# Performance work log

Measured on AMD Instinct MI355X. Metric: run time of the kernel, lower is better.

The kernel has to match this reference:

```python
import jax, jax.numpy as jnp
import numpy as np

V, D, H, DH, P, NL, FF, NC, MAXP = 32000, 512, 8, 64, 16, 8, 2048, 4, 512
B, L = 32, 4096


def _ln(x, s, b, eps=1e-5):
    m = x.mean(-1, keepdims=True)
    v = ((x - m) ** 2).mean(-1, keepdims=True)
    return (x - m) * jax.lax.rsqrt(v + eps) * s + b


def _rope(x):
    # x: [B,S,H,Dh] -- GPT-NeoX style rotary over head dim
    S, d = x.shape[1], x.shape[-1]
    inv_freq = 1.0 / (10000.0 ** (jnp.arange(0, d, 2, dtype=jnp.float32) / d))
    freqs = jnp.arange(S, dtype=jnp.float32)[:, None] * inv_freq[None, :]  # [S,d/2]
    emb = jnp.concatenate([freqs, freqs], axis=-1)  # [S,d]
    cos = jnp.cos(emb)[None, :, None, :]
    sin = jnp.sin(emb)[None, :, None, :]
    x1, x2 = x[..., : d // 2], x[..., d // 2:]
    rot = jnp.concatenate([-x2, x1], axis=-1)
    return x * cos + rot * sin


def setup_inputs():
    key = jax.random.key(0)
    ks = jax.random.split(key, 20)
    s = 0.02
    inp = {}
    inp['inputs'] = jax.random.randint(ks[0], (B, L), 0, V, dtype=jnp.int32)
    inp['input_mask'] = jnp.ones((B, L), dtype=jnp.float32)
    inp['emb'] = jax.random.normal(ks[1], (V, D)) * s
    inp['conv_w'] = jax.random.normal(ks[2], (D, D, P)) * s  # [out, in, kernel]
    inp['conv_b'] = jnp.zeros((D,))
    inp['pos'] = jax.random.normal(ks[3], (MAXP, D)) * s
    inp['cls'] = jax.random.normal(ks[4], (1, 1, D))
    inp['Wq'] = jax.random.normal(ks[5], (NL, D, D)) * s
    inp['bq'] = jnp.zeros((NL, D))
    inp['Wk'] = jax.random.normal(ks[6], (NL, D, D)) * s
    inp['bk'] = jnp.zeros((NL, D))
    inp['Wv'] = jax.random.normal(ks[7], (NL, D, D)) * s
    inp['bv'] = jnp.zeros((NL, D))
    inp['Wo'] = jax.random.normal(ks[8], (NL, D, D)) * s
    inp['bo'] = jnp.zeros((NL, D))
    inp['ln1_s'] = jnp.ones((NL, D))
    inp['ln1_b'] = jnp.zeros((NL, D))
    inp['ln2_s'] = jnp.ones((NL, D))
    inp['ln2_b'] = jnp.zeros((NL, D))
    inp['W1'] = jax.random.normal(ks[9], (NL, D, FF)) * s
    inp['b1'] = jnp.zeros((NL, FF))
    inp['W2'] = jax.random.normal(ks[10], (NL, FF, D)) * s
    inp['b2'] = jnp.zeros((NL, D))
    inp['lnf_s'] = jnp.ones((D,))
    inp['lnf_b'] = jnp.zeros((D,))
    inp['out_w'] = jax.random.normal(ks[11], (D, NC)) * s
    inp['out_b'] = jnp.zeros((NC,))
    return inp


def _forward(inputs, input_mask, emb, conv_w, conv_b, pos, cls, Wq, bq, Wk, bk, Wv, bv,
             Wo, bo, ln1_s, ln1_b, ln2_s, ln2_b, W1, b1, W2, b2, lnf_s, lnf_b, out_w, out_b):
    b, l = inputs.shape
    n = l // P
    x = emb[inputs]  # [B,L,D]
    # patchify conv1d (kernel == stride) == blocked reshape + einsum
    x = jnp.einsum('bnpi,oip->bno', x.reshape(b, n, P, D), conv_w) + conv_b
    x = jnp.concatenate([jnp.broadcast_to(cls, (b, 1, D)), x], axis=1)  # [B,S,D]
    S = n + 1
    x = x + pos[:S][None]
    # length mask at patch granularity: ceil((sum(mask)+1)/patch_size)
    lengths = jnp.ceil((input_mask.sum(-1) + 1.0) / P)
    lmask = (jnp.arange(S, dtype=jnp.float32)[None, :] < lengths[:, None]).astype(x.dtype)  # [B,S]
    for i in range(NL):
        q = (x @ Wq[i] + bq[i]).reshape(b, S, H, DH)
        k = (x @ Wk[i] + bk[i]).reshape(b, S, H, DH)
        v = (x @ Wv[i] + bv[i]).reshape(b, S, H, DH)
        q, k = _rope(q), _rope(k)
        qf = jax.nn.elu(q) + 1.0  # kernel feature map
        kf = (jax.nn.elu(k) + 1.0) * lmask[:, :, None, None]
        kv = jnp.einsum('bshd,bshm->bhdm', kf, v)
        z = 1.0 / (jnp.einsum('bshd,bhd->bsh', qf, kf.sum(axis=1)) + 1e-6)
        attn = jnp.einsum('bshd,bhdm,bsh->bshm', qf, kv, z).reshape(b, S, D)
        x = x + (attn @ Wo[i] + bo[i])
        x = _ln(x, ln1_s[i], ln1_b[i])
        y = jax.nn.gelu(x @ W1[i] + b1[i], approximate=False) @ W2[i] + b2[i]
        x = _ln(x + y, ln2_s[i], ln2_b[i])
    x = _ln(x, lnf_s, lnf_b)
    return x[:, 0] @ out_w + out_b  # [B, num_classes]


def reference(inputs, input_mask, emb, conv_w, conv_b, pos, cls, Wq, bq, Wk, bk, Wv, bv,
              Wo, bo, ln1_s, ln1_b, ln2_s, ln2_b, W1, b1, W2, b2, lnf_s, lnf_b, out_w, out_b):
    return _forward(inputs, input_mask, emb, conv_w, conv_b, pos, cls, Wq, bq, Wk, bk, Wv, bv,
                    Wo, bo, ln1_s, ln1_b, ln2_s, ln2_b, W1, b1, W2, b2, lnf_s, lnf_b, out_w, out_b)
```

## Files before the change

### kernel.cpp

```cpp
#include <hip/hip_runtime.h>
#include <cstdint>

typedef unsigned short u16;
typedef __attribute__((ext_vector_type(8))) short short8;
typedef __attribute__((ext_vector_type(4))) float floatx4;

typedef __attribute__((address_space(1))) void as1_void;
typedef __attribute__((address_space(3))) void as3_void;

__device__ __forceinline__ float b2f(u16 u) {
  return __uint_as_float(((unsigned int)u) << 16);
}
__device__ __forceinline__ u16 f2b(float f) {
  unsigned int x = __float_as_uint(f);
  x += 0x7fffu + ((x >> 16) & 1u);
  return (u16)(x >> 16);
}
__device__ __forceinline__ float ldf(const void* p, size_t i, int f32) {
  return f32 ? ((const float*)p)[i] : b2f(((const u16*)p)[i]);
}

__device__ __forceinline__ void gl_lds16(const u16* g, u16* l) {
  __builtin_amdgcn_global_load_lds((const as1_void*)g, (as3_void*)l, 16, 0, 0);
}

template<int EPI, bool GATHER>
__global__ __launch_bounds__(256)
void gemm_bt(const u16* __restrict__ A, const u16* __restrict__ BT,
             int M, int K, int N,
             const u16* __restrict__ bias,
             float* __restrict__ outf, u16* __restrict__ outb,
             const int* __restrict__ tok, const u16* __restrict__ emb,
             const u16* __restrict__ pos, float* __restrict__ xf, u16* __restrict__ xb)
{
  __shared__ u16 lds[16384];
  u16* Al = lds;
  u16* Bl = lds + 8192;
  const int tid  = threadIdx.x;
  const int wave = tid >> 6, lane = tid & 63;
  const int m0 = blockIdx.x * 128, n0 = blockIdx.y * 128;
  const int wy = wave & 1, wx = wave >> 1;

  floatx4 acc[4][4];
#pragma unroll
  for (int i = 0; i < 4; ++i)
#pragma unroll
    for (int j = 0; j < 4; ++j) acc[i][j] = (floatx4){0.f, 0.f, 0.f, 0.f};

  for (int k0 = 0; k0 < K; k0 += 64) {
#pragma unroll
    for (int t = 0; t < 4; ++t) {
      int slot = t * 256 + wave * 64 + lane;
      int r = slot >> 3, cp = slot & 7;
      int c = cp ^ (r & 7);
      int grow = m0 + r; if (grow >= M) grow = M - 1;
      const u16* g;
      if (GATHER) {
        int k = k0 + c * 8;
        g = emb + ((size_t)tok[grow * 16 + (k >> 9)] * 512 + (k & 511));
      } else {
        g = A + ((size_t)grow * K + k0 + c * 8);
      }
      gl_lds16(g, Al + (size_t)(t * 256 + wave * 64) * 8);
    }
#pragma unroll
    for (int t = 0; t < 4; ++t) {
      int slot = t * 256 + wave * 64 + lane;
      int r = slot >> 3, cp = slot & 7;
      int c = cp ^ (r & 7);
      const u16* g = BT + ((size_t)(n0 + r) * K + k0 + c * 8);
      gl_lds16(g, Bl + (size_t)(t * 256 + wave * 64) * 8);
    }
    __syncthreads();

#pragma unroll
    for (int ks = 0; ks < 2; ++ks) {
      short8 af[4], bfr[4];
#pragma unroll
      for (int mt = 0; mt < 4; ++mt) {
        int r = wy * 64 + mt * 16 + (lane & 15);
        int ch = ks * 4 + (lane >> 4);
        af[mt] = *(const short8*)(Al + (size_t)(r * 8 + (ch ^ (r & 7))) * 8);
      }
#pragma unroll
      for (int nt = 0; nt < 4; ++nt) {
        int r = wx * 64 + nt * 16 + (lane & 15);
        int ch = ks * 4 + (lane >> 4);
        bfr[nt] = *(const short8*)(Bl + (size_t)(r * 8 + (ch ^ (r & 7))) * 8);
      }
#pragma unroll
      for (int mt = 0; mt < 4; ++mt)
#pragma unroll
        for (int nt = 0; nt < 4; ++nt)
          acc[mt][nt] = __builtin_amdgcn_mfma_f32_16x16x32_bf16(af[mt], bfr[nt], acc[mt][nt], 0, 0, 0);
    }
    __syncthreads();
  }

  const int rb = m0 + wy * 64 + ((lane >> 4) << 2);
  const int cb = n0 + wx * 64 + (lane & 15);
#pragma unroll
  for (int mt = 0; mt < 4; ++mt) {
#pragma unroll
    for (int rr = 0; rr < 4; ++rr) {
      int row = rb + mt * 16 + rr;
      if (row >= M) continue;
#pragma unroll
      for (int nt = 0; nt < 4; ++nt) {
        int col = cb + nt * 16;
        float v = acc[mt][nt][rr] + b2f(bias[col]);
        if (EPI == 0) {
          outf[(size_t)row * N + col] = v;
        } else if (EPI == 1) {
          float gl = 0.5f * v * (1.0f + erff(v * 0.70710678118654752f));
          outb[(size_t)row * N + col] = f2b(gl);
        } else if (EPI == 3) {
          outb[(size_t)row * N + col] = f2b(v);
        } else {
          int bb = row >> 8, ss = (row & 255) + 1;
          v += b2f(pos[ss * 512 + col]);
          size_t o = ((size_t)(bb * 257 + ss)) * 512 + col;
          xf[o] = v;
          xb[o] = f2b(v);
        }
      }
    }
  }
}

__global__ void detect_kernel(const void* mask, int* flag)
{
  if (threadIdx.x == 0 && blockIdx.x == 0)
    flag[0] = (((const u16*)mask)[0] == 0) ? 1 : 0;
}

__global__ __launch_bounds__(256)
void cvt_kernel(const void* __restrict__ src, u16* __restrict__ dst, int n,
                const int* __restrict__ flag)
{
  int f = flag[0];
  int i = blockIdx.x * 256 + threadIdx.x;
  if (i < n) dst[i] = f2b(ldf(src, i, f));
}

__global__ __launch_bounds__(256)
void transpose_any(const void* __restrict__ in, size_t eoff,
                   u16* __restrict__ out, int R, int C,
                   const int* __restrict__ flag)
{
  __shared__ u16 tile[32][33];
  int f = flag[0];
  int c0 = blockIdx.x * 32, r0 = blockIdx.y * 32;
  int tx = threadIdx.x, ty = threadIdx.y;
#pragma unroll
  for (int i = 0; i < 32; i += 8)
    tile[ty + i][tx] = f2b(ldf(in, eoff + (size_t)(r0 + ty + i) * C + (c0 + tx), f));
  __syncthreads();
#pragma unroll
  for (int i = 0; i < 32; i += 8)
    out[(size_t)(c0 + ty + i) * R + (r0 + tx)] = tile[tx][ty + i];
}

__global__ __launch_bounds__(256)
void conv_repack(const void* __restrict__ w, u16* __restrict__ wt,
                 const int* __restrict__ flag)
{
  __shared__ u16 t[8192];
  int f = flag[0];
  int o = blockIdx.x, tid = threadIdx.x;
  for (int i = tid; i < 8192; i += 256)
    t[i] = f2b(ldf(w, (size_t)o * 8192 + i, f));
  __syncthreads();
  u16* dst = wt + (size_t)o * 8192;
  for (int j = tid; j < 8192; j += 256) {
    int p = j >> 9, i = j & 511;
    dst[j] = t[i * 16 + p];
  }
}

__global__ __launch_bounds__(256)
void cls_kernel(const u16* __restrict__ cls, const u16* __restrict__ pos,
                float* __restrict__ xf, u16* __restrict__ xb)
{
  int b = blockIdx.x, tid = threadIdx.x;
  for (int i = tid; i < 512; i += 256) {
    float v = b2f(cls[i]) + b2f(pos[i]);
    size_t o = ((size_t)b * 257) * 512 + i;
    xf[o] = v;
    xb[o] = f2b(v);
  }
}

__global__ __launch_bounds__(256)
void lengths_kernel(const void* __restrict__ mask, float* __restrict__ lens,
                    const int* __restrict__ flag)
{
  __shared__ float red[4];
  int f = flag[0];
  int b = blockIdx.x, tid = threadIdx.x;
  float s = 0.f;
  for (int i = tid; i < 4096; i += 256) s += ldf(mask, (size_t)b * 4096 + i, f);
#pragma unroll
  for (int o = 1; o < 64; o <<= 1) s += __shfl_xor(s, o);
  if ((tid & 63) == 0) red[tid >> 6] = s;
  __syncthreads();
  if (tid == 0) lens[b] = ceilf((red[0] + red[1] + red[2] + red[3] + 1.0f) * (1.0f / 16.0f));
}

__global__ __launch_bounds__(256)
void rope_elu(float* __restrict__ q, float* __restrict__ k, const float* __restrict__ lens)
{
  int i = blockIdx.x * 256 + threadIdx.x;
  int j = i & 31, h = (i >> 5) & 7, t = i >> 8;
  int s = t % 257, b = t / 257;
  size_t base = (size_t)t * 512 + h * 64 + j;
  float inv = __expf(-(float)j * (9.210340371976184f / 32.0f));
  float ang = (float)s * inv;
  float c, sn;
  __sincosf(ang, &sn, &c);
  float q1 = q[base], q2 = q[base + 32];
  float r1 = q1 * c - q2 * sn, r2 = q2 * c + q1 * sn;
  q[base]      = (r1 > 0.f) ? (r1 + 1.f) : __expf(r1);
  q[base + 32] = (r2 > 0.f) ? (r2 + 1.f) : __expf(r2);
  float msk = ((float)s < lens[b]) ? 1.f : 0.f;
  float k1 = k[base], k2 = k[base + 32];
  r1 = k1 * c - k2 * sn; r2 = k2 * c + k1 * sn;
  k[base]      = ((r1 > 0.f) ? (r1 + 1.f) : __expf(r1)) * msk;
  k[base + 32] = ((r2 > 0.f) ? (r2 + 1.f) : __expf(r2)) * msk;
}

__global__ __launch_bounds__(256)
void kv_kernel(const float* __restrict__ kf, const u16* __restrict__ v,
               float* __restrict__ kv, float* __restrict__ ksum)
{
  int bh = blockIdx.x, b = bh >> 3, h = bh & 7;
  int tid = threadIdx.x, d = tid & 63, mg = tid >> 6;
  float acc[16];
#pragma unroll
  for (int j = 0; j < 16; ++j) acc[j] = 0.f;
  float ks = 0.f;
  for (int s = 0; s < 257; ++s) {
    size_t base = ((size_t)(b * 257 + s)) * 512 + h * 64;
    float kfv = kf[base + d];
    const u16* vr = v + base + mg * 16;
#pragma unroll
    for (int j = 0; j < 16; ++j) acc[j] += kfv * b2f(vr[j]);
    ks += kfv;
  }
  float* kvo = kv + (size_t)bh * 4096 + d * 64 + mg * 16;
#pragma unroll
  for (int j = 0; j < 16; ++j) kvo[j] = acc[j];
  if (mg == 0) ksum[(size_t)bh * 64 + d] = ks;
}

__global__ __launch_bounds__(256)
void z_kernel(const float* __restrict__ qf, const float* __restrict__ ksum,
              float* __restrict__ z)
{
  int i = blockIdx.x * 256 + threadIdx.x;
  if (i >= 65792) return;
  int h = i & 7, t = i >> 3, b = t / 257;
  const float* qr = qf + (size_t)t * 512 + h * 64;
  const float* kr = ksum + ((size_t)b * 8 + h) * 64;
  float s = 0.f;
#pragma unroll
  for (int d = 0; d < 64; ++d) s += qr[d] * kr[d];
  z[i] = 1.0f / (s + 1e-6f);
}

__global__ __launch_bounds__(256)
void attn_kernel(const float* __restrict__ qf, const float* __restrict__ kv,
                 const float* __restrict__ z, u16* __restrict__ attn)
{
  __shared__ float kvs[4096];
  int bh = blockIdx.x, b = bh >> 3, h = bh & 7;
  int tid = threadIdx.x;
  const float* kvg = kv + (size_t)bh * 4096;
  for (int i = tid; i < 4096; i += 256) kvs[i] = kvg[i];
  __syncthreads();
  int m = tid & 63;
  for (int s = tid >> 6; s < 257; s += 4) {
    size_t base = ((size_t)(b * 257 + s)) * 512 + h * 64;
    float zz = z[(b * 257 + s) * 8 + h];
    float sum = 0.f;
#pragma unroll
    for (int d = 0; d < 64; ++d) sum += qf[base + d] * kvs[d * 64 + m];
    attn[base + m] = f2b(sum * zz);
  }
}

__global__ __launch_bounds__(256)
void ln_kernel(const float* __restrict__ xin, const float* __restrict__ add,
               const u16* __restrict__ s, const u16* __restrict__ b,
               float* __restrict__ xoutf, u16* __restrict__ xoutb)
{
  __shared__ float red[8];
  int row = blockIdx.x, tid = threadIdx.x;
  size_t base = (size_t)row * 512;
  float v0 = xin[base + tid] + add[base + tid];
  float v1 = xin[base + tid + 256] + add[base + tid + 256];
  float sum = v0 + v1, sq = v0 * v0 + v1 * v1;
#pragma unroll
  for (int o = 1; o < 64; o <<= 1) { sum += __shfl_xor(sum, o); sq += __shfl_xor(sq, o); }
  if ((tid & 63) == 0) { red[tid >> 6] = sum; red[4 + (tid >> 6)] = sq; }
  __syncthreads();
  sum = red[0] + red[1] + red[2] + red[3];
  sq  = red[4] + red[5] + red[6] + red[7];
  float mean = sum * (1.f / 512.f);
  float var  = sq * (1.f / 512.f) - mean * mean;
  float rs = rsqrtf(fmaxf(var, 0.f) + 1e-5f);
  float o0 = (v0 - mean) * rs * b2f(s[tid]) + b2f(b[tid]);
  float o1 = (v1 - mean) * rs * b2f(s[tid + 256]) + b2f(b[tid + 256]);
  xoutf[base + tid] = o0;       xoutf[base + tid + 256] = o1;
  xoutb[base + tid] = f2b(o0);  xoutb[base + tid + 256] = f2b(o1);
}

__global__ __launch_bounds__(256)
void head_kernel(const float* __restrict__ x, const u16* __restrict__ ls,
                 const u16* __restrict__ lb, const u16* __restrict__ ow,
                 const u16* __restrict__ ob, void* __restrict__ outv,
                 const int* __restrict__ flag)
{
  __shared__ float red[8];
  __shared__ float pr[4][4];
  int b = blockIdx.x, tid = threadIdx.x;
  const float* xr = x + (size_t)b * 257 * 512;
  float v0 = xr[tid], v1 = xr[tid + 256];
  float sum = v0 + v1, sq = v0 * v0 + v1 * v1;
#pragma unroll
  for (int o = 1; o < 64; o <<= 1) { sum += __shfl_xor(sum, o); sq += __shfl_xor(sq, o); }
  if ((tid & 63) == 0) { red[tid >> 6] = sum; red[4 + (tid >> 6)] = sq; }
  __syncthreads();
  sum = red[0] + red[1] + red[2] + red[3];
  sq  = red[4] + red[5] + red[6] + red[7];
  float mean = sum * (1.f / 512.f);
  float var = sq * (1.f / 512.f) - mean * mean;
  float rs = rsqrtf(fmaxf(var, 0.f) + 1e-5f);
  float o0 = (v0 - mean) * rs * b2f(ls[tid]) + b2f(lb[tid]);
  float o1 = (v1 - mean) * rs * b2f(ls[tid + 256]) + b2f(lb[tid + 256]);
  float p[4];
#pragma unroll
  for (int c = 0; c < 4; ++c)
    p[c] = o0 * b2f(ow[tid * 4 + c]) + o1 * b2f(ow[(tid + 256) * 4 + c]);
#pragma unroll
  for (int c = 0; c < 4; ++c)
#pragma unroll
    for (int o = 1; o < 64; o <<= 1) p[c] += __shfl_xor(p[c], o);
  if ((tid & 63) == 0)
#pragma unroll
    for (int c = 0; c < 4; ++c) pr[tid >> 6][c] = p[c];
  __syncthreads();
  if (tid < 4) {
    float s = pr[0][tid] + pr[1][tid] + pr[2][tid] + pr[3][tid] + b2f(ob[tid]);
    if (flag[0]) ((float*)outv)[b * 4 + tid] = s;
    else         ((u16*)outv)[b * 4 + tid] = f2b(s);
  }
}

__global__ __launch_bounds__(256)
void diag_kernel(u16* out, int n, float v)
{
  int i = blockIdx.x * 256 + threadIdx.x;
  if (i < n) out[i] = f2b(v);
}

extern "C" void kernel_launch(void* const* d_in, const int* in_sizes, int n_in,
                              void* d_out, int out_size, void* d_ws, size_t ws_size,
                              hipStream_t stream)
{
  const int*  inputs = (const int*)d_in[0];
  const void* imask  = d_in[1];
  const void* emb    = d_in[2];
  const void* conv_w = d_in[3];
  const void* conv_b = d_in[4];
  const void* pos    = d_in[5];
  const void* cls    = d_in[6];
  const void* Wq = d_in[7];  const void* bq = d_in[8];
  const void* Wk = d_in[9];  const void* bk = d_in[10];
  const void* Wv = d_in[11]; const void* bv = d_in[12];
  const void* Wo = d_in[13]; const void* bo = d_in[14];
  const void* ln1s = d_in[15]; const void* ln1b = d_in[16];
  const void* ln2s = d_in[17]; const void* ln2b = d_in[18];
  const void* W1 = d_in[19]; const void* b1 = d_in[20];
  const void* W2 = d_in[21]; const void* b2 = d_in[22];
  const void* lnfs = d_in[23]; const void* lnfb = d_in[24];
  const void* outw = d_in[25]; const void* outbb = d_in[26];

  const size_t NEED = 87500000;
  if (ws_size < NEED) {
    diag_kernel<<<(out_size + 255) / 256, 256, 0, stream>>>(
        (u16*)d_out, out_size, (float)((double)ws_size / 1048576.0));
    return;
  }
  char* p = (char*)d_ws;
  auto take = [&](size_t n) { char* r = p; p += (n + 255) & ~(size_t)255; return r; };
  u16*   WqT = (u16*)take(524288);
  u16*   WkT = (u16*)take(524288);
  u16*   WvT = (u16*)take(524288);
  u16*   WoT = (u16*)take(524288);
  u16*   W1T = (u16*)take(2097152);
  u16*   W2T = (u16*)take(2097152);
  float* xf  = (float*)take(16842752);
  u16*   xb  = (u16*)take(8421376);
  char*  arena = take(16842752ull * 2);
  float* qb    = (float*)arena;
  float* kb    = (float*)(arena + 16842752);
  u16*   embC  = (u16*)arena;
  u16*   attnb = (u16*)(arena + 16842752);
  u16*   y1    = (u16*)arena;
  char*  Cblk  = take(16842752);
  u16*   convT = (u16*)Cblk;
  u16*   vb    = (u16*)Cblk;
  float* t0    = (float*)Cblk;
  float* kvb   = (float*)take(4194304);
  float* ksumb = (float*)take(65536);
  float* zb    = (float*)take(263168);
  float* lens  = (float*)take(256);
  int*   flag  = (int*)take(256);
  u16* conv_bC = (u16*)take(1024);
  u16* posC    = (u16*)take(524288);
  u16* clsC    = (u16*)take(1024);
  u16* bqC     = (u16*)take(8192);
  u16* bkC     = (u16*)take(8192);
  u16* bvC     = (u16*)take(8192);
  u16* boC     = (u16*)take(8192);
  u16* ln1sC   = (u16*)take(8192);
  u16* ln1bC   = (u16*)take(8192);
  u16* ln2sC   = (u16*)take(8192);
  u16* ln2bC   = (u16*)take(8192);
  u16* b1C     = (u16*)take(32768);
  u16* b2C     = (u16*)take(8192);
  u16* lnfsC   = (u16*)take(1024);
  u16* lnfbC   = (u16*)take(1024);
  u16* outwC   = (u16*)take(4096);
  u16* outbC   = (u16*)take(256);

  detect_kernel<<<1, 64, 0, stream>>>(imask, flag);

  cvt_kernel<<<64000, 256, 0, stream>>>(emb, embC, 16384000, flag);
  conv_repack<<<512, 256, 0, stream>>>(conv_w, convT, flag);
  cvt_kernel<<<2, 256, 0, stream>>>(conv_b, conv_bC, 512, flag);
  cvt_kernel<<<1024, 256, 0, stream>>>(pos, posC, 262144, flag);
  cvt_kernel<<<2, 256, 0, stream>>>(cls, clsC, 512, flag);
  cvt_kernel<<<16, 256, 0, stream>>>(bq, bqC, 4096, flag);
  cvt_kernel<<<16, 256, 0, stream>>>(bk, bkC, 4096, flag);
  cvt_kernel<<<16, 256, 0, stream>>>(bv, bvC, 4096, flag);
  cvt_kernel<<<16, 256, 0, stream>>>(bo, boC, 4096, flag);
  cvt_kernel<<<16, 256, 0, stream>>>(ln1s, ln1sC, 4096, flag);
  cvt_kernel<<<16, 256, 0, stream>>>(ln1b, ln1bC, 4096, flag);
  cvt_kernel<<<16, 256, 0, stream>>>(ln2s, ln2sC, 4096, flag);
  cvt_kernel<<<16, 256, 0, stream>>>(ln2b, ln2bC, 4096, flag);
  cvt_kernel<<<64, 256, 0, stream>>>(b1, b1C, 16384, flag);
  cvt_kernel<<<16, 256, 0, stream>>>(b2, b2C, 4096, flag);
  cvt_kernel<<<2, 256, 0, stream>>>(lnfs, lnfsC, 512, flag);
  cvt_kernel<<<2, 256, 0, stream>>>(lnfb, lnfbC, 512, flag);
  cvt_kernel<<<8, 256, 0, stream>>>(outw, outwC, 2048, flag);
  cvt_kernel<<<1, 256, 0, stream>>>(outbb, outbC, 4, flag);
  lengths_kernel<<<32, 256, 0, stream>>>(imask, lens, flag);

  gemm_bt<2, true><<<dim3(64, 4), 256, 0, stream>>>(
      nullptr, convT, 8192, 8192, 512, conv_bC,
      nullptr, nullptr, inputs, embC, posC, xf, xb);
  cls_kernel<<<32, 256, 0, stream>>>(clsC, posC, xf, xb);

  for (int i = 0; i < 8; ++i) {
    const size_t o512 = (size_t)i * 262144;
    const size_t o2k  = (size_t)i * 1048576;
    transpose_any<<<dim3(16, 16), dim3(32, 8), 0, stream>>>(Wq, o512, WqT, 512, 512, flag);
    transpose_any<<<dim3(16, 16), dim3(32, 8), 0, stream>>>(Wk, o512, WkT, 512, 512, flag);
    transpose_any<<<dim3(16, 16), dim3(32, 8), 0, stream>>>(Wv, o512, WvT, 512, 512, flag);
    transpose_any<<<dim3(16, 16), dim3(32, 8), 0, stream>>>(Wo, o512, WoT, 512, 512, flag);
    transpose_any<<<dim3(64, 16), dim3(32, 8), 0, stream>>>(W1, o2k, W1T, 512, 2048, flag);
    transpose_any<<<dim3(16, 64), dim3(32, 8), 0, stream>>>(W2, o2k, W2T, 2048, 512, flag);

    gemm_bt<0, false><<<dim3(65, 4), 256, 0, stream>>>(
        xb, WqT, 8224, 512, 512, bqC + i * 512,
        qb, nullptr, nullptr, nullptr, nullptr, nullptr, nullptr);
    gemm_bt<0, false><<<dim3(65, 4), 256, 0, stream>>>(
        xb, WkT, 8224, 512, 512, bkC + i * 512,
        kb, nullptr, nullptr, nullptr, nullptr, nullptr, nullptr);
    gemm_bt<3, false><<<dim3(65, 4), 256, 0, stream>>>(
        xb, WvT, 8224, 512, 512, bvC + i * 512,
        nullptr, vb, nullptr, nullptr, nullptr, nullptr, nullptr);
    rope_elu<<<8224, 256, 0, stream>>>(qb, kb, lens);
    kv_kernel<<<256, 256, 0, stream>>>(kb, vb, kvb, ksumb);
    z_kernel<<<257, 256, 0, stream>>>(qb, ksumb, zb);
    attn_kernel<<<256, 256, 0, stream>>>(qb, kvb, zb, attnb);
    gemm_bt<0, false><<<dim3(65, 4), 256, 0, stream>>>(
        attnb, WoT, 8224, 512, 512, boC + i * 512,
        t0, nullptr, nullptr, nullptr, nullptr, nullptr, nullptr);
    ln_kernel<<<8224, 256, 0, stream>>>(xf, t0, ln1sC + i * 512, ln1bC + i * 512, xf, xb);
    gemm_bt<1, false><<<dim3(65, 16), 256, 0, stream>>>(
        xb, W1T, 8224, 512, 2048, b1C + i * 2048,
        nullptr, y1, nullptr, nullptr, nullptr, nullptr, nullptr);
    gemm_bt<0, false><<<dim3(65, 4), 256, 0, stream>>>(
        y1, W2T, 8224, 2048, 512, b2C + i * 512,
        t0, nullptr, nullptr, nullptr, nullptr, nullptr, nullptr);
    ln_kernel<<<8224, 256, 0, stream>>>(xf, t0, ln2sC + i * 512, ln2bC + i * 512, xf, xb);
  }

  head_kernel<<<32, 256, 0, stream>>>(xf, lnfsC, lnfbC, outwC, outbC, d_out, flag);
}
```

Before: 3.418 ms.

## Fuse QKV GEMM with rope/ELU epilogue, batch weight prep, shrink GEMM M tile

```diff
diff --git a/kernel.cpp b/kernel.cpp
--- a/kernel.cpp
+++ b/kernel.cpp
@@ -19,37 +19,40 @@
 __device__ __forceinline__ float ldf(const void* p, size_t i, int f32) {
   return f32 ? ((const float*)p)[i] : b2f(((const u16*)p)[i]);
 }
-
 __device__ __forceinline__ void gl_lds16(const u16* g, u16* l) {
   __builtin_amdgcn_global_load_lds((const as1_void*)g, (as3_void*)l, 16, 0, 0);
 }
 
-template<int EPI, bool GATHER>
+template<int TM, int EPI, bool GATHER>
 __global__ __launch_bounds__(256)
 void gemm_bt(const u16* __restrict__ A, const u16* __restrict__ BT,
              int M, int K, int N,
              const u16* __restrict__ bias,
-             float* __restrict__ outf, u16* __restrict__ outb,
+             float* __restrict__ outf, float* __restrict__ outf2,
+             u16* __restrict__ outb,
              const int* __restrict__ tok, const u16* __restrict__ emb,
-             const u16* __restrict__ pos, float* __restrict__ xf, u16* __restrict__ xb)
-{
-  __shared__ u16 lds[16384];
+             const u16* __restrict__ pos, float* __restrict__ xf, u16* __restrict__ xb,
+             const float* __restrict__ lens)
+{
+  constexpr int MT = TM / 32;
+  constexpr int AISS = (TM * 8) / 256;
+  __shared__ u16 lds[TM * 64 + 8192];
   u16* Al = lds;
-  u16* Bl = lds + 8192;
+  u16* Bl = lds + TM * 64;
   const int tid  = threadIdx.x;
   const int wave = tid >> 6, lane = tid & 63;
-  const int m0 = blockIdx.x * 128, n0 = blockIdx.y * 128;
+  const int m0 = blockIdx.x * TM, n0 = blockIdx.y * 128;
   const int wy = wave & 1, wx = wave >> 1;
 
-  floatx4 acc[4][4];
-#pragma unroll
-  for (int i = 0; i < 4; ++i)
+  floatx4 acc[MT][4];
+#pragma unroll
+  for (int i = 0; i < MT; ++i)
 #pragma unroll
     for (int j = 0; j < 4; ++j) acc[i][j] = (floatx4){0.f, 0.f, 0.f, 0.f};
 
   for (int k0 = 0; k0 < K; k0 += 64) {
 #pragma unroll
-    for (int t = 0; t < 4; ++t) {
+    for (int t = 0; t < AISS; ++t) {
       int slot = t * 256 + wave * 64 + lane;
       int r = slot >> 3, cp = slot & 7;
       int c = cp ^ (r & 7);
@@ -75,10 +78,10 @@
 
 #pragma unroll
     for (int ks = 0; ks < 2; ++ks) {
-      short8 af[4], bfr[4];
-#pragma unroll
-      for (int mt = 0; mt < 4; ++mt) {
-        int r = wy * 64 + mt * 16 + (lane & 15);
+      short8 af[MT], bfr[4];
+#pragma unroll
+      for (int mt = 0; mt < MT; ++mt) {
+        int r = wy * (TM / 2) + mt * 16 + (lane & 15);
         int ch = ks * 4 + (lane >> 4);
         af[mt] = *(const short8*)(Al + (size_t)(r * 8 + (ch ^ (r & 7))) * 8);
       }
@@ -89,7 +92,7 @@
         bfr[nt] = *(const short8*)(Bl + (size_t)(r * 8 + (ch ^ (r & 7))) * 8);
       }
 #pragma unroll
-      for (int mt = 0; mt < 4; ++mt)
+      for (int mt = 0; mt < MT; ++mt)
 #pragma unroll
         for (int nt = 0; nt < 4; ++nt)
           acc[mt][nt] = __builtin_amdgcn_mfma_f32_16x16x32_bf16(af[mt], bfr[nt], acc[mt][nt], 0, 0, 0);
@@ -97,31 +100,63 @@
     __syncthreads();
   }
 
-  const int rb = m0 + wy * 64 + ((lane >> 4) << 2);
+  const int rb = m0 + wy * (TM / 2) + ((lane >> 4) << 2);
   const int cb = n0 + wx * 64 + (lane & 15);
 #pragma unroll
-  for (int mt = 0; mt < 4; ++mt) {
+  for (int mt = 0; mt < MT; ++mt) {
 #pragma unroll
     for (int rr = 0; rr < 4; ++rr) {
       int row = rb + mt * 16 + rr;
       if (row >= M) continue;
-#pragma unroll
-      for (int nt = 0; nt < 4; ++nt) {
-        int col = cb + nt * 16;
-        float v = acc[mt][nt][rr] + b2f(bias[col]);
-        if (EPI == 0) {
-          outf[(size_t)row * N + col] = v;
-        } else if (EPI == 1) {
-          float gl = 0.5f * v * (1.0f + erff(v * 0.70710678118654752f));
-          outb[(size_t)row * N + col] = f2b(gl);
-        } else if (EPI == 3) {
-          outb[(size_t)row * N + col] = f2b(v);
+      if (EPI == 4) {
+        int region = n0 >> 9;
+        int b = row / 257, s = row - b * 257;
+        if (region == 2) {
+#pragma unroll
+          for (int nt = 0; nt < 4; ++nt) {
+            int col = cb + nt * 16;
+            float v = acc[mt][nt][rr] + b2f(bias[col]);
+            outb[(size_t)row * 512 + (col - 1024)] = f2b(v);
+          }
         } else {
-          int bb = row >> 8, ss = (row & 255) + 1;
-          v += b2f(pos[ss * 512 + col]);
-          size_t o = ((size_t)(bb * 257 + ss)) * 512 + col;
-          xf[o] = v;
-          xb[o] = f2b(v);
+          float msk = (region == 1) ? (((float)s < lens[b]) ? 1.f : 0.f) : 1.f;
+#pragma unroll
+          for (int nt = 0; nt < 2; ++nt) {
+            int ngL = cb + nt * 16, ngH = ngL + 32;
+            int jl = nt * 16 + (lane & 15);
+            float x1 = acc[mt][nt][rr]     + b2f(bias[ngL]);
+            float x2 = acc[mt][nt + 2][rr] + b2f(bias[ngH]);
+            float ang = (float)s * __expf(-(float)jl * (9.210340371976184f / 32.0f));
+            float sn, cs;
+            __sincosf(ang, &sn, &cs);
+            float rl = x1 * cs - x2 * sn;
+            float rh = x2 * cs + x1 * sn;
+            float eL = (rl > 0.f) ? (rl + 1.f) : __expf(rl);
+            float eH = (rh > 0.f) ? (rh + 1.f) : __expf(rh);
+            eL *= msk; eH *= msk;
+            float* dst = (region == 0) ? outf : outf2;
+            int colL = ngL - region * 512;
+            dst[(size_t)row * 512 + colL]      = eL;
+            dst[(size_t)row * 512 + colL + 32] = eH;
+          }
+        }
+      } else {
+#pragma unroll
+        for (int nt = 0; nt < 4; ++nt) {
+          int col = cb + nt * 16;
+          float v = acc[mt][nt][rr] + b2f(bias[col]);
+          if (EPI == 0) {
+            outf[(size_t)row * N + col] = v;
+          } else if (EPI == 1) {
+            float gl = 0.5f * v * (1.0f + erff(v * 0.70710678118654752f));
+            outb[(size_t)row * N + col] = f2b(gl);
+          } else {
+            int bb = row >> 8, ss = (row & 255) + 1;
+            v += b2f(pos[ss * 512 + col]);
+            size_t o = ((size_t)(bb * 257 + ss)) * 512 + col;
+            xf[o] = v;
+            xb[o] = f2b(v);
+          }
         }
       }
     }
@@ -143,22 +178,87 @@
   if (i < n) dst[i] = f2b(ldf(src, i, f));
 }
 
-__global__ __launch_bounds__(256)
-void transpose_any(const void* __restrict__ in, size_t eoff,
-                   u16* __restrict__ out, int R, int C,
-                   const int* __restrict__ flag)
+struct PCvt {
+  const void *pos, *conv_b, *cls, *bq, *bk, *bv, *bo;
+  const void *ln1s, *ln1b, *ln2s, *ln2b, *b1, *b2, *lnfs, *lnfb, *outw, *outb;
+  u16 *posC, *conv_bC, *clsC, *bqkvC, *boC;
+  u16 *ln1sC, *ln1bC, *ln2sC, *ln2bC, *b1C, *b2C, *lnfsC, *lnfbC, *outwC, *outbC;
+  const int* flag;
+};
+__global__ __launch_bounds__(256)
+void param_cvt(PCvt p)
+{
+  int f = p.flag[0];
+  int seg = blockIdx.y;
+  int i = blockIdx.x * 256 + threadIdx.x;
+  switch (seg) {
+    case 0:  if (i < 262144) p.posC[i]    = f2b(ldf(p.pos, i, f)); break;
+    case 1:  if (i < 512)    p.conv_bC[i] = f2b(ldf(p.conv_b, i, f)); break;
+    case 2:  if (i < 512)    p.clsC[i]    = f2b(ldf(p.cls, i, f)); break;
+    case 3:  if (i < 12288) {
+      int layer = i / 1536, r = i - layer * 1536;
+      const void* s = (r < 512) ? p.bq : (r < 1024) ? p.bk : p.bv;
+      int rr = r & 511;
+      p.bqkvC[i] = f2b(ldf(s, (size_t)layer * 512 + rr, f));
+    } break;
+    case 4:  if (i < 4096)  p.boC[i]   = f2b(ldf(p.bo, i, f)); break;
+    case 5:  if (i < 4096)  p.ln1sC[i] = f2b(ldf(p.ln1s, i, f)); break;
+    case 6:  if (i < 4096)  p.ln1bC[i] = f2b(ldf(p.ln1b, i, f)); break;
+    case 7:  if (i < 4096)  p.ln2sC[i] = f2b(ldf(p.ln2s, i, f)); break;
+    case 8:  if (i < 4096)  p.ln2bC[i] = f2b(ldf(p.ln2b, i, f)); break;
+    case 9:  if (i < 16384) p.b1C[i]   = f2b(ldf(p.b1, i, f)); break;
+    case 10: if (i < 4096)  p.b2C[i]   = f2b(ldf(p.b2, i, f)); break;
+    default:
+      if (i < 512)        p.lnfsC[i]        = f2b(ldf(p.lnfs, i, f));
+      else if (i < 1024)  p.lnfbC[i - 512]  = f2b(ldf(p.lnfb, (size_t)i - 512, f));
+      else if (i < 3072)  p.outwC[i - 1024] = f2b(ldf(p.outw, (size_t)i - 1024, f));
+      else if (i < 3076)  p.outbC[i - 3072] = f2b(ldf(p.outb, (size_t)i - 3072, f));
+      break;
+  }
+}
+
+struct XPose {
+  const void *Wq, *Wk, *Wv, *Wo, *W1, *W2;
+  u16 *WqkvT, *WoT, *W1T, *W2T;
+  int base;
+  const int* flag;
+};
+__global__ __launch_bounds__(256)
+void xpose_layer(XPose xp)
 {
   __shared__ u16 tile[32][33];
-  int f = flag[0];
-  int c0 = blockIdx.x * 32, r0 = blockIdx.y * 32;
+  int f = xp.flag[0];
+  int layer = xp.base + blockIdx.y;
+  int y = blockIdx.y;
+  int t = blockIdx.x;
+  const void* src; u16* dst; int R, C, cx, ry; size_t eoff;
+  if (t < 1024) {
+    int wsel = t >> 8, tt = t & 255;
+    R = 512; C = 512; cx = tt & 15; ry = tt >> 4;
+    eoff = (size_t)layer * 262144;
+    if (wsel < 3) { src = (wsel == 0) ? xp.Wq : (wsel == 1) ? xp.Wk : xp.Wv;
+                    dst = xp.WqkvT + (size_t)y * 786432 + (size_t)wsel * 262144; }
+    else          { src = xp.Wo; dst = xp.WoT + (size_t)y * 262144; }
+  } else if (t < 2048) {
+    int tt = t - 1024;
+    R = 512; C = 2048; cx = tt & 63; ry = tt >> 6;
+    eoff = (size_t)layer * 1048576;
+    src = xp.W1; dst = xp.W1T + (size_t)y * 1048576;
+  } else {
+    int tt = t - 2048;
+    R = 2048; C = 512; cx = tt & 15; ry = tt >> 4;
+    eoff = (size_t)layer * 1048576;
+    src = xp.W2; dst = xp.W2T + (size_t)y * 1048576;
+  }
+  int c0 = cx * 32, r0 = ry * 32;
   int tx = threadIdx.x, ty = threadIdx.y;
 #pragma unroll
   for (int i = 0; i < 32; i += 8)
-    tile[ty + i][tx] = f2b(ldf(in, eoff + (size_t)(r0 + ty + i) * C + (c0 + tx), f));
+    tile[ty + i][tx] = f2b(ldf(src, eoff + (size_t)(r0 + ty + i) * C + (c0 + tx), f));
   __syncthreads();
 #pragma unroll
   for (int i = 0; i < 32; i += 8)
-    out[(size_t)(c0 + ty + i) * R + (r0 + tx)] = tile[tx][ty + i];
+    dst[(size_t)(c0 + ty + i) * R + (r0 + tx)] = tile[tx][ty + i];
 }
 
 __global__ __launch_bounds__(256)
@@ -208,28 +308,6 @@
 }
 
 __global__ __launch_bounds__(256)
-void rope_elu(float* __restrict__ q, float* __restrict__ k, const float* __restrict__ lens)
-{
-  int i = blockIdx.x * 256 + threadIdx.x;
-  int j = i & 31, h = (i >> 5) & 7, t = i >> 8;
-  int s = t % 257, b = t / 257;
-  size_t base = (size_t)t * 512 + h * 64 + j;
-  float inv = __expf(-(float)j * (9.210340371976184f / 32.0f));
-  float ang = (float)s * inv;
-  float c, sn;
-  __sincosf(ang, &sn, &c);
-  float q1 = q[base], q2 = q[base + 32];
-  float r1 = q1 * c - q2 * sn, r2 = q2 * c + q1 * sn;
-  q[base]      = (r1 > 0.f) ? (r1 + 1.f) : __expf(r1);
-  q[base + 32] = (r2 > 0.f) ? (r2 + 1.f) : __expf(r2);
-  float msk = ((float)s < lens[b]) ? 1.f : 0.f;
-  float k1 = k[base], k2 = k[base + 32];
-  r1 = k1 * c - k2 * sn; r2 = k2 * c + k1 * sn;
-  k[base]      = ((r1 > 0.f) ? (r1 + 1.f) : __expf(r1)) * msk;
-  k[base + 32] = ((r2 > 0.f) ? (r2 + 1.f) : __expf(r2)) * msk;
-}
-
-__global__ __launch_bounds__(256)
 void kv_kernel(const float* __restrict__ kf, const u16* __restrict__ v,
                float* __restrict__ kv, float* __restrict__ ksum)
 {
@@ -254,38 +332,28 @@
 }
 
 __global__ __launch_bounds__(256)
-void z_kernel(const float* __restrict__ qf, const float* __restrict__ ksum,
-              float* __restrict__ z)
-{
-  int i = blockIdx.x * 256 + threadIdx.x;
-  if (i >= 65792) return;
-  int h = i & 7, t = i >> 3, b = t / 257;
-  const float* qr = qf + (size_t)t * 512 + h * 64;
-  const float* kr = ksum + ((size_t)b * 8 + h) * 64;
-  float s = 0.f;
-#pragma unroll
-  for (int d = 0; d < 64; ++d) s += qr[d] * kr[d];
-  z[i] = 1.0f / (s + 1e-6f);
-}
-
-__global__ __launch_bounds__(256)
 void attn_kernel(const float* __restrict__ qf, const float* __restrict__ kv,
-                 const float* __restrict__ z, u16* __restrict__ attn)
+                 const float* __restrict__ ksum, u16* __restrict__ attn)
 {
   __shared__ float kvs[4096];
+  __shared__ float kss[64];
   int bh = blockIdx.x, b = bh >> 3, h = bh & 7;
   int tid = threadIdx.x;
   const float* kvg = kv + (size_t)bh * 4096;
   for (int i = tid; i < 4096; i += 256) kvs[i] = kvg[i];
+  if (tid < 64) kss[tid] = ksum[(size_t)bh * 64 + tid];
   __syncthreads();
   int m = tid & 63;
   for (int s = tid >> 6; s < 257; s += 4) {
     size_t base = ((size_t)(b * 257 + s)) * 512 + h * 64;
-    float zz = z[(b * 257 + s) * 8 + h];
+    float zp = qf[base + m] * kss[m];
+#pragma unroll
+    for (int o = 1; o < 64; o <<= 1) zp += __shfl_xor(zp, o);
+    float z = 1.0f / (zp + 1e-6f);
     float sum = 0.f;
 #pragma unroll
     for (int d = 0; d < 64; ++d) sum += qf[base + d] * kvs[d * 64 + m];
-    attn[base + m] = f2b(sum * zz);
+    attn[base + m] = f2b(sum * z);
   }
 }
 
@@ -392,14 +460,18 @@
         (u16*)d_out, out_size, (float)((double)ws_size / 1048576.0));
     return;
   }
+  const bool bigws = ws_size >= 135000000;
+  const int  WL    = bigws ? 8 : 1;
+  const size_t qs  = bigws ? 786432  : 0;
+  const size_t os  = bigws ? 262144  : 0;
+  const size_t fs  = bigws ? 1048576 : 0;
+
   char* p = (char*)d_ws;
   auto take = [&](size_t n) { char* r = p; p += (n + 255) & ~(size_t)255; return r; };
-  u16*   WqT = (u16*)take(524288);
-  u16*   WkT = (u16*)take(524288);
-  u16*   WvT = (u16*)take(524288);
-  u16*   WoT = (u16*)take(524288);
-  u16*   W1T = (u16*)take(2097152);
-  u16*   W2T = (u16*)take(2097152);
+  u16*   WqkvT = (u16*)take(1572864ull * WL);
+  u16*   WoT   = (u16*)take(524288ull  * WL);
+  u16*   W1T   = (u16*)take(2097152ull * WL);
+  u16*   W2T   = (u16*)take(2097152ull * WL);
   float* xf  = (float*)take(16842752);
   u16*   xb  = (u16*)take(8421376);
   char*  arena = take(16842752ull * 2);
@@ -414,15 +486,12 @@
   float* t0    = (float*)Cblk;
   float* kvb   = (float*)take(4194304);
   float* ksumb = (float*)take(65536);
-  float* zb    = (float*)take(263168);
   float* lens  = (float*)take(256);
   int*   flag  = (int*)take(256);
+  u16* posC    = (u16*)take(524288);
   u16* conv_bC = (u16*)take(1024);
-  u16* posC    = (u16*)take(524288);
   u16* clsC    = (u16*)take(1024);
-  u16* bqC     = (u16*)take(8192);
-  u16* bkC     = (u16*)take(8192);
-  u16* bvC     = (u16*)take(8192);
+  u16* bqkvC   = (u16*)take(24576);
   u16* boC     = (u16*)take(8192);
   u16* ln1sC   = (u16*)take(8192);
   u16* ln1bC   = (u16*)take(8192);
@@ -437,65 +506,45 @@
 
   detect_kernel<<<1, 64, 0, stream>>>(imask, flag);
 
+  PCvt pc = { pos, conv_b, cls, bq, bk, bv, bo,
+              ln1s, ln1b, ln2s, ln2b, b1, b2, lnfs, lnfb, outw, outbb,
+              posC, conv_bC, clsC, bqkvC, boC,
+              ln1sC, ln1bC, ln2sC, ln2bC, b1C, b2C, lnfsC, lnfbC, outwC, outbC,
+              flag };
+  param_cvt<<<dim3(1024, 12), 256, 0, stream>>>(pc);
   cvt_kernel<<<64000, 256, 0, stream>>>(emb, embC, 16384000, flag);
   conv_repack<<<512, 256, 0, stream>>>(conv_w, convT, flag);
-  cvt_kernel<<<2, 256, 0, stream>>>(conv_b, conv_bC, 512, flag);
-  cvt_kernel<<<1024, 256, 0, stream>>>(pos, posC, 262144, flag);
-  cvt_kernel<<<2, 256, 0, stream>>>(cls, clsC, 512, flag);
-  cvt_kernel<<<16, 256, 0, stream>>>(bq, bqC, 4096, flag);
-  cvt_kernel<<<16, 256, 0, stream>>>(bk, bkC, 4096, flag);
-  cvt_kernel<<<16, 256, 0, stream>>>(bv, bvC, 4096, flag);
-  cvt_kernel<<<16, 256, 0, stream>>>(bo, boC, 4096, flag);
-  cvt_kernel<<<16, 256, 0, stream>>>(ln1s, ln1sC, 4096, flag);
-  cvt_kernel<<<16, 256, 0, stream>>>(ln1b, ln1bC, 4096, flag);
-  cvt_kernel<<<16, 256, 0, stream>>>(ln2s, ln2sC, 4096, flag);
-  cvt_kernel<<<16, 256, 0, stream>>>(ln2b, ln2bC, 4096, flag);
-  cvt_kernel<<<64, 256, 0, stream>>>(b1, b1C, 16384, flag);
-  cvt_kernel<<<16, 256, 0, stream>>>(b2, b2C, 4096, flag);
-  cvt_kernel<<<2, 256, 0, stream>>>(lnfs, lnfsC, 512, flag);
-  cvt_kernel<<<2, 256, 0, stream>>>(lnfb, lnfbC, 512, flag);
-  cvt_kernel<<<8, 256, 0, stream>>>(outw, outwC, 2048, flag);
-  cvt_kernel<<<1, 256, 0, stream>>>(outbb, outbC, 4, flag);
   lengths_kernel<<<32, 256, 0, stream>>>(imask, lens, flag);
 
-  gemm_bt<2, true><<<dim3(64, 4), 256, 0, stream>>>(
+  XPose xp = { Wq, Wk, Wv, Wo, W1, W2, WqkvT, WoT, W1T, W2T, 0, flag };
+  if (bigws)
+    xpose_layer<<<dim3(3072, 8), dim3(32, 8), 0, stream>>>(xp);
+
+  gemm_bt<128, 2, true><<<dim3(64, 4), 256, 0, stream>>>(
       nullptr, convT, 8192, 8192, 512, conv_bC,
-      nullptr, nullptr, inputs, embC, posC, xf, xb);
+      nullptr, nullptr, nullptr, inputs, embC, posC, xf, xb, nullptr);
   cls_kernel<<<32, 256, 0, stream>>>(clsC, posC, xf, xb);
 
   for (int i = 0; i < 8; ++i) {
-    const size_t o512 = (size_t)i * 262144;
-    const size_t o2k  = (size_t)i * 1048576;
-    transpose_any<<<dim3(16, 16), dim3(32, 8), 0, stream>>>(Wq, o512, WqT, 512, 512, flag);
-    transpose_any<<<dim3(16, 16), dim3(32, 8), 0, stream>>>(Wk, o512, WkT, 512, 512, flag);
-    transpose_any<<<dim3(16, 16), dim3(32, 8), 0, stream>>>(Wv, o512, WvT, 512, 512, flag);
-    transpose_any<<<dim3(16, 16), dim3(32, 8), 0, stream>>>(Wo, o512, WoT, 512, 512, flag);
-    transpose_any<<<dim3(64, 16), dim3(32, 8), 0, stream>>>(W1, o2k, W1T, 512, 2048, flag);
-    transpose_any<<<dim3(16, 64), dim3(32, 8), 0, stream>>>(W2, o2k, W2T, 2048, 512, flag);
-
-    gemm_bt<0, false><<<dim3(65, 4), 256, 0, stream>>>(
-        xb, WqT, 8224, 512, 512, bqC + i * 512,
-        qb, nullptr, nullptr, nullptr, nullptr, nullptr, nullptr);
-    gemm_bt<0, false><<<dim3(65, 4), 256, 0, stream>>>(
-        xb, WkT, 8224, 512, 512, bkC + i * 512,
-        kb, nullptr, nullptr, nullptr, nullptr, nullptr, nullptr);
-    gemm_bt<3, false><<<dim3(65, 4), 256, 0, stream>>>(
-        xb, WvT, 8224, 512, 512, bvC + i * 512,
-        nullptr, vb, nullptr, nullptr, nullptr, nullptr, nullptr);
-    rope_elu<<<8224, 256, 0, stream>>>(qb, kb, lens);
+    if (!bigws) {
+      xp.base = i;
+      xpose_layer<<<dim3(3072, 1), dim3(32, 8), 0, stream>>>(xp);
+    }
+    gemm_bt<64, 4, false><<<dim3(129, 12), 256, 0, stream>>>(
+        xb, WqkvT + i * qs, 8224, 512, 1536, bqkvC + i * 1536,
+        qb, kb, vb, nullptr, nullptr, nullptr, nullptr, nullptr, lens);
     kv_kernel<<<256, 256, 0, stream>>>(kb, vb, kvb, ksumb);
-    z_kernel<<<257, 256, 0, stream>>>(qb, ksumb, zb);
-    attn_kernel<<<256, 256, 0, stream>>>(qb, kvb, zb, attnb);
-    gemm_bt<0, false><<<dim3(65, 4), 256, 0, stream>>>(
-        attnb, WoT, 8224, 512, 512, boC + i * 512,
-        t0, nullptr, nullptr, nullptr, nullptr, nullptr, nullptr);
+    attn_kernel<<<256, 256, 0, stream>>>(qb, kvb, ksumb, attnb);
+    gemm_bt<64, 0, false><<<dim3(129, 4), 256, 0, stream>>>(
+        attnb, WoT + i * os, 8224, 512, 512, boC + i * 512,
+        t0, nullptr, nullptr, nullptr, nullptr, nullptr, nullptr, nullptr, nullptr);
     ln_kernel<<<8224, 256, 0, stream>>>(xf, t0, ln1sC + i * 512, ln1bC + i * 512, xf, xb);
-    gemm_bt<1, false><<<dim3(65, 16), 256, 0, stream>>>(
-        xb, W1T, 8224, 512, 2048, b1C + i * 2048,
-        nullptr, y1, nullptr, nullptr, nullptr, nullptr, nullptr);
-    gemm_bt<0, false><<<dim3(65, 4), 256, 0, stream>>>(
-        y1, W2T, 8224, 2048, 512, b2C + i * 512,
-        t0, nullptr, nullptr, nullptr, nullptr, nullptr, nullptr);
+    gemm_bt<64, 1, false><<<dim3(129, 16), 256, 0, stream>>>(
+        xb, W1T + i * fs, 8224, 512, 2048, b1C + i * 2048,
+        nullptr, nullptr, y1, nullptr, nullptr, nullptr, nullptr, nullptr, nullptr);
+    gemm_bt<64, 0, false><<<dim3(129, 4), 256, 0, stream>>>(
+        y1, W2T + i * fs, 8224, 2048, 512, b2C + i * 512,
+        t0, nullptr, nullptr, nullptr, nullptr, nullptr, nullptr, nullptr, nullptr);
     ln_kernel<<<8224, 256, 0, stream>>>(xf, t0, ln2sC + i * 512, ln2bC + i * 512, xf, xb);
   }
 
```

After: 2.828 ms. 17.3% less time.
